# Kernel tuning notes

Measured on AMD Instinct MI355X. Metric: run time of the kernel, lower is better.

## Reference

```python
import jax, jax.numpy as jnp
import numpy as np

N, K_IN, K_OUT = 200000, 8, 4
E, D, H, O = 800000, 64, 128, 1


def setup_inputs() -> dict:
    key = jax.random.key(0)
    ks = jax.random.split(key, 8)
    edges = jax.random.normal(ks[0], (E, D), dtype=jnp.float32)
    in_idx = jax.random.randint(ks[1], (N, K_IN), 0, E, dtype=jnp.int32)
    in_mask = jax.random.randint(ks[2], (N, K_IN), 0, 2, dtype=jnp.int32)
    out_idx = jax.random.randint(ks[3], (N, K_OUT), 0, E, dtype=jnp.int32)
    out_mask = jax.random.randint(ks[4], (N, K_OUT), 0, 2, dtype=jnp.int32)
    # FC stack params: layer0 takes 2*D (edge feat ++ pooled attention context)
    W0 = jax.random.normal(ks[5], (H, 2 * D), dtype=jnp.float32) * (1.0 / np.sqrt(2 * D))
    b0 = jnp.zeros((H,), dtype=jnp.float32)
    W1 = jax.random.normal(ks[6], (H, H), dtype=jnp.float32) * (1.0 / np.sqrt(H))
    b1 = jnp.zeros((H,), dtype=jnp.float32)
    Wout = jax.random.normal(ks[7], (O, H), dtype=jnp.float32) * (1.0 / np.sqrt(H))
    bout = jnp.zeros((O,), dtype=jnp.float32)
    return {"edges": edges, "in_idx": in_idx, "in_mask": in_mask,
            "out_idx": out_idx, "out_mask": out_mask,
            "W0": W0, "b0": b0, "W1": W1, "b1": b1, "Wout": Wout, "bout": bout}


def _forward(edges, in_idx, in_mask, out_idx, out_mask, W0, b0, W1, b1, Wout, bout):
    d = edges.shape[1]
    mbool = in_mask.astype(bool)                       # [N, K_in]
    mf = in_mask.astype(edges.dtype)[..., None]        # [N, K_in, 1]
    # gather per-node in-edge sets: [N, K_in, D]
    Ein = edges[in_idx]
    # self-attention over the in-edge set (query=key=value=in_edges)
    scores = jnp.einsum('nqd,nkd->nqk', Ein, Ein) / jnp.sqrt(jnp.asarray(d, edges.dtype))
    scores = jnp.where(mbool[:, None, :], scores, jnp.asarray(-1e9, edges.dtype))
    attn = jax.nn.softmax(scores, axis=-1)
    att_out = jnp.einsum('nqk,nkd->nqd', attn, Ein)    # [N, K_in, D]
    # pool attended rows over valid queries -> weighted_in_edges [N, D]
    denom = jnp.maximum(mf.sum(axis=1), 1.0)
    pooled = (att_out * mf).sum(axis=1) / denom
    # per out-edge: concat(edge_feat, pooled) -> MLP
    Eout = edges[out_idx]                              # [N, K_out, D]
    pooled_b = jnp.broadcast_to(pooled[:, None, :], Eout.shape)
    x = jnp.concatenate([Eout, pooled_b], axis=-1)     # [N, K_out, 2D]
    h = jax.nn.relu(jnp.einsum('nkd,hd->nkh', x, W0) + b0)
    h = jax.nn.relu(jnp.einsum('nkh,gh->nkg', h, W1) + b1)
    y = jnp.einsum('nkh,oh->nko', h, Wout) + bout      # [N, K_out, O]
    y = y * out_mask.astype(y.dtype)[..., None]        # zero padded out-edges
    return y.reshape(-1, y.shape[-1])                  # [N*K_out, O]


def reference(edges, in_idx, in_mask, out_idx, out_mask, W0, b0, W1, b1, Wout, bout):
    return _forward(edges, in_idx, in_mask, out_idx, out_mask, W0, b0, W1, b1, Wout, bout)
```

## Files before the change

### kernel.cpp

```cpp
#include <hip/hip_runtime.h>
#include <math.h>

#define D 64
#define H 128
#define KIN 8
#define KOUT 4
#define NPB 16
#define ROWS (NPB*KOUT)
#define THREADS 256
#define WAVES 4
#define NPW (NPB/WAVES)
#define XLDB 136
#define ELD16 72

typedef __attribute__((ext_vector_type(8))) short short8v;
typedef __attribute__((ext_vector_type(4))) float f32x4;

__device__ inline unsigned short f2bf(float f) {
    union { float f; unsigned u; } v; v.f = f;
    unsigned r = v.u + 0x7FFF + ((v.u >> 16) & 1);
    return (unsigned short)(r >> 16);
}

__global__ void convert_w_kernel(const float* __restrict__ W0,
                                 const float* __restrict__ W1,
                                 unsigned short* __restrict__ Wbf) {
    const int i = blockIdx.x * 256 + threadIdx.x;
    const float v = (i < H*H) ? W0[i] : W1[i - H*H];
    Wbf[i] = f2bf(v);
}

__global__ __launch_bounds__(THREADS, 4) void encoder_kernel(
    const float* __restrict__ edges,
    const int*   __restrict__ in_idx,
    const int*   __restrict__ in_mask,
    const int*   __restrict__ out_idx,
    const int*   __restrict__ out_mask,
    const float* __restrict__ b0, const float* __restrict__ b1,
    const float* __restrict__ Wout, const float* __restrict__ bout,
    const unsigned short* __restrict__ Wbf,
    float* __restrict__ out, int N)
{
    __shared__ __align__(16) unsigned short xbuf[ROWS][XLDB];
    __shared__ __align__(16) unsigned short eins[WAVES][16][ELD16];
    __shared__ float omaskf[ROWS];

    const int tid  = threadIdx.x;
    const int wave = tid >> 6;
    const int lane = tid & 63;
    const int nodeBase = blockIdx.x * NPB;

    const int col = lane & 15;
    const int grp = lane >> 4;

    for (int it = 0; it < 2; ++it) {
        const int nl0 = wave * NPW + it * 2;
        const int n0  = nodeBase + nl0;

        const int   idx_l  = in_idx [n0*KIN  + col];
        const float mkcol  = (float)in_mask[n0*KIN  + col];
        const int   oidx_l = out_idx[n0*KOUT + (lane & 7)];

        float ein_r[16];
        #pragma unroll
        for (int r = 0; r < 16; ++r) {
            const int gi = __shfl(idx_l, r);
            ein_r[r] = edges[(size_t)gi * D + lane];
            eins[wave][r][lane] = f2bf(ein_r[r]);
        }
        #pragma unroll
        for (int r = 0; r < 8; ++r) {
            const int gi = __shfl(oidx_l, r);
            xbuf[nl0*KOUT + r][lane] = f2bf(edges[(size_t)gi * D + lane]);
        }
        if (lane < 2*KOUT) omaskf[nl0*KOUT + lane] = (float)out_mask[n0*KOUT + lane];

        const short8v f0 = *(const short8v*)&eins[wave][col][grp*8];
        const short8v f1 = *(const short8v*)&eins[wave][col][32 + grp*8];
        f32x4 sc = (f32x4){0.f, 0.f, 0.f, 0.f};
        sc = __builtin_amdgcn_mfma_f32_16x16x32_bf16(f0, f0, sc, 0, 0, 0);
        sc = __builtin_amdgcn_mfma_f32_16x16x32_bf16(f1, f1, sc, 0, 0, 0);

        float s0, s1, s2, s3;
        {
            const bool kv = (mkcol > 0.f);
            #define MSK(jj, sv) { const int row = grp*4 + jj; \
                const bool ok = kv && ((row < 8) == (col < 8)); \
                sv = ok ? sc[jj] * 0.125f : -1e9f; }
            MSK(0, s0) MSK(1, s1) MSK(2, s2) MSK(3, s3)
            #undef MSK
        }
        float m0=s0, m1=s1, m2=s2, m3=s3;
        #pragma unroll
        for (int off = 1; off < 16; off <<= 1) {
            m0 = fmaxf(m0, __shfl_xor(m0, off));
            m1 = fmaxf(m1, __shfl_xor(m1, off));
            m2 = fmaxf(m2, __shfl_xor(m2, off));
            m3 = fmaxf(m3, __shfl_xor(m3, off));
        }
        float e0=__expf(s0-m0), e1=__expf(s1-m1), e2=__expf(s2-m2), e3=__expf(s3-m3);
        float t0=e0, t1=e1, t2=e2, t3=e3;
        #pragma unroll
        for (int off = 1; off < 16; off <<= 1) {
            t0 += __shfl_xor(t0, off); t1 += __shfl_xor(t1, off);
            t2 += __shfl_xor(t2, off); t3 += __shfl_xor(t3, off);
        }
        float wsum = __shfl(mkcol, grp*4 + 0) * (e0 / t0)
                   + __shfl(mkcol, grp*4 + 1) * (e1 / t1)
                   + __shfl(mkcol, grp*4 + 2) * (e2 / t2)
                   + __shfl(mkcol, grp*4 + 3) * (e3 / t3);
        wsum += __shfl_xor(wsum, 16);
        wsum += __shfl_xor(wsum, 32);

        float dn = mkcol;
        dn += __shfl_xor(dn, 1); dn += __shfl_xor(dn, 2); dn += __shfl_xor(dn, 4);
        const float dnA = fmaxf(__shfl(dn, 0), 1.f);
        const float dnB = fmaxf(__shfl(dn, 8), 1.f);

        float pA = 0.f, pB = 0.f;
        #pragma unroll
        for (int k = 0; k < 8; ++k) {
            pA += __shfl(wsum, k)     * ein_r[k];
            pB += __shfl(wsum, 8 + k) * ein_r[8 + k];
        }
        const unsigned short pbA = f2bf(pA / dnA);
        const unsigned short pbB = f2bf(pB / dnB);
        #pragma unroll
        for (int j = 0; j < KOUT; ++j) {
            xbuf[ nl0   *KOUT + j][D + lane] = pbA;
            xbuf[(nl0+1)*KOUT + j][D + lane] = pbB;
        }
    }
    __syncthreads();

    const int rowbase = (wave >> 1) * 32;
    const int colbase = (wave & 1) * 64;
    const int l15  = lane & 15;
    const int kofs = (lane >> 4) * 8;
    const int rrow = (lane >> 4) * 4;

    #pragma unroll
    for (int layer = 0; layer < 2; ++layer) {
        const unsigned short* __restrict__ Wl = Wbf + layer * (H*H);
        const float* __restrict__ bl = layer ? b1 : b0;

        f32x4 acc[2][4];
        #pragma unroll
        for (int ct = 0; ct < 4; ++ct) {
            const float bv = bl[colbase + ct*16 + l15];
            #pragma unroll
            for (int r = 0; r < 2; ++r) acc[r][ct] = (f32x4){bv, bv, bv, bv};
        }

        #pragma unroll
        for (int ks = 0; ks < 4; ++ks) {
            short8v bf[4];
            #pragma unroll
            for (int ct = 0; ct < 4; ++ct)
                bf[ct] = *(const short8v*)&Wl[(size_t)(colbase + ct*16 + l15) * H + ks*32 + kofs];
            #pragma unroll
            for (int r = 0; r < 2; ++r) {
                const short8v a = *(const short8v*)&xbuf[rowbase + r*16 + l15][ks*32 + kofs];
                #pragma unroll
                for (int ct = 0; ct < 4; ++ct)
                    acc[r][ct] = __builtin_amdgcn_mfma_f32_16x16x32_bf16(a, bf[ct], acc[r][ct], 0, 0, 0);
            }
        }
        __syncthreads();
        #pragma unroll
        for (int r = 0; r < 2; ++r)
            #pragma unroll
            for (int ct = 0; ct < 4; ++ct)
                #pragma unroll
                for (int j = 0; j < 4; ++j)
                    xbuf[rowbase + r*16 + rrow + j][colbase + ct*16 + l15] =
                        f2bf(fmaxf(acc[r][ct][j], 0.f));
        __syncthreads();
    }

    {
        const int row = tid >> 2;
        const int kq  = tid & 3;
        float p = 0.f;
        #pragma unroll
        for (int m = 0; m < 4; ++m) {
            const int k0 = kq*32 + m*8;
            const short8v hv = *(const short8v*)&xbuf[row][k0];
            const float4 w0 = *(const float4*)&Wout[k0];
            const float4 w1 = *(const float4*)&Wout[k0 + 4];
            union { unsigned u; float f; } c;
            float acc8 = 0.f;
            c.u = ((unsigned)(unsigned short)hv[0]) << 16; acc8 += c.f * w0.x;
            c.u = ((unsigned)(unsigned short)hv[1]) << 16; acc8 += c.f * w0.y;
            c.u = ((unsigned)(unsigned short)hv[2]) << 16; acc8 += c.f * w0.z;
            c.u = ((unsigned)(unsigned short)hv[3]) << 16; acc8 += c.f * w0.w;
            c.u = ((unsigned)(unsigned short)hv[4]) << 16; acc8 += c.f * w1.x;
            c.u = ((unsigned)(unsigned short)hv[5]) << 16; acc8 += c.f * w1.y;
            c.u = ((unsigned)(unsigned short)hv[6]) << 16; acc8 += c.f * w1.z;
            c.u = ((unsigned)(unsigned short)hv[7]) << 16; acc8 += c.f * w1.w;
            p += acc8;
        }
        p += __shfl_xor(p, 1);
        p += __shfl_xor(p, 2);
        if (kq == 0) {
            const long long grow = (long long)nodeBase * KOUT + row;
            if (grow < (long long)N * KOUT)
                out[grow] = (p + bout[0]) * omaskf[row];
        }
    }
}

extern "C" void kernel_launch(void* const* d_in, const int* in_sizes, int n_in,
                              void* d_out, int out_size, void* d_ws, size_t ws_size,
                              hipStream_t stream)
{
    const float* edges  = (const float*)d_in[0];
    const int* in_idx   = (const int*)d_in[1];
    const int* in_mask  = (const int*)d_in[2];
    const int* out_idx  = (const int*)d_in[3];
    const int* out_mask = (const int*)d_in[4];
    const float* W0   = (const float*)d_in[5];
    const float* b0   = (const float*)d_in[6];
    const float* W1   = (const float*)d_in[7];
    const float* b1   = (const float*)d_in[8];
    const float* Wout = (const float*)d_in[9];
    const float* bout = (const float*)d_in[10];
    float* out = (float*)d_out;
    unsigned short* Wbf = (unsigned short*)d_ws;

    const int nNodes = in_sizes[1] / KIN;
    convert_w_kernel<<<(2*H*H + 255) / 256, 256, 0, stream>>>(W0, W1, Wbf);
    const int grid = (nNodes + NPB - 1) / NPB;
    encoder_kernel<<<grid, THREADS, 0, stream>>>(
        edges, in_idx, in_mask, out_idx, out_mask,
        b0, b1, Wout, bout, Wbf, out, nNodes);
}
```

Baseline: 643.7 us.

## Make each wave own its 16 MLP rows, removing block barriers and batching gathers

Each wave now handles its 4 nodes end to end. It keeps a private 16-row activation tile and computes all 128 output columns itself, so every __syncthreads in the MLP stage is gone. All 48 edge-row gathers are issued up front before any compute to expose more memory-level parallelism. Occupancy is raised via launch bounds and a smaller LDS stride. The trade-offs are that each wave loads the full weight matrices from global/L2 with no sharing across waves, and more registers are live during the gathers.

```diff
diff --git a/kernel.cpp b/kernel.cpp
--- a/kernel.cpp
+++ b/kernel.cpp
@@ -5,12 +5,9 @@
 #define H 128
 #define KIN 8
 #define KOUT 4
-#define NPB 16
-#define ROWS (NPB*KOUT)
 #define THREADS 256
 #define WAVES 4
-#define NPW (NPB/WAVES)
-#define XLDB 136
+#define XLDB 132
 #define ELD16 72
 
 typedef __attribute__((ext_vector_type(8))) short short8v;
@@ -30,7 +27,7 @@
     Wbf[i] = f2bf(v);
 }
 
-__global__ __launch_bounds__(THREADS, 4) void encoder_kernel(
+__global__ __launch_bounds__(THREADS, 6) void encoder_kernel(
     const float* __restrict__ edges,
     const int*   __restrict__ in_idx,
     const int*   __restrict__ in_mask,
@@ -41,40 +38,37 @@
     const unsigned short* __restrict__ Wbf,
     float* __restrict__ out, int N)
 {
-    __shared__ __align__(16) unsigned short xbuf[ROWS][XLDB];
+    __shared__ __align__(16) unsigned short xbuf[WAVES][16][XLDB];
     __shared__ __align__(16) unsigned short eins[WAVES][16][ELD16];
-    __shared__ float omaskf[ROWS];
 
     const int tid  = threadIdx.x;
     const int wave = tid >> 6;
     const int lane = tid & 63;
-    const int nodeBase = blockIdx.x * NPB;
-
-    const int col = lane & 15;
-    const int grp = lane >> 4;
-
-    for (int it = 0; it < 2; ++it) {
-        const int nl0 = wave * NPW + it * 2;
-        const int n0  = nodeBase + nl0;
-
-        const int   idx_l  = in_idx [n0*KIN  + col];
-        const float mkcol  = (float)in_mask[n0*KIN  + col];
-        const int   oidx_l = out_idx[n0*KOUT + (lane & 7)];
-
-        float ein_r[16];
-        #pragma unroll
-        for (int r = 0; r < 16; ++r) {
-            const int gi = __shfl(idx_l, r);
-            ein_r[r] = edges[(size_t)gi * D + lane];
-            eins[wave][r][lane] = f2bf(ein_r[r]);
-        }
-        #pragma unroll
-        for (int r = 0; r < 8; ++r) {
-            const int gi = __shfl(oidx_l, r);
-            xbuf[nl0*KOUT + r][lane] = f2bf(edges[(size_t)gi * D + lane]);
-        }
-        if (lane < 2*KOUT) omaskf[nl0*KOUT + lane] = (float)out_mask[n0*KOUT + lane];
-
+    const int col  = lane & 15;
+    const int grp  = lane >> 4;
+    const int n0   = blockIdx.x * 16 + wave * 4;
+
+    const int   idxA = in_idx [(size_t)(n0+0)*KIN + col];
+    const int   idxB = in_idx [(size_t)(n0+2)*KIN + col];
+    const float mkA  = (float)in_mask[(size_t)(n0+0)*KIN + col];
+    const float mkB  = (float)in_mask[(size_t)(n0+2)*KIN + col];
+    const int   oidx = out_idx[(size_t)n0*KOUT + col];
+    const float omsk = (float)out_mask[(size_t)n0*KOUT + (lane >> 2)];
+
+    float einA[16], einB[16], eout[16];
+    #pragma unroll
+    for (int r = 0; r < 16; ++r) einA[r] = edges[(size_t)__shfl(idxA, r) * D + lane];
+    #pragma unroll
+    for (int r = 0; r < 16; ++r) einB[r] = edges[(size_t)__shfl(idxB, r) * D + lane];
+    #pragma unroll
+    for (int r = 0; r < 16; ++r) eout[r] = edges[(size_t)__shfl(oidx, r) * D + lane];
+
+    #pragma unroll
+    for (int r = 0; r < 16; ++r) xbuf[wave][r][lane] = f2bf(eout[r]);
+
+    auto do_pair = [&](const float* einr, const float mkcol, const int xrow0) {
+        #pragma unroll
+        for (int r = 0; r < 16; ++r) eins[wave][r][lane] = f2bf(einr[r]);
         const short8v f0 = *(const short8v*)&eins[wave][col][grp*8];
         const short8v f1 = *(const short8v*)&eins[wave][col][32 + grp*8];
         f32x4 sc = (f32x4){0.f, 0.f, 0.f, 0.f};
@@ -120,72 +114,56 @@
         float pA = 0.f, pB = 0.f;
         #pragma unroll
         for (int k = 0; k < 8; ++k) {
-            pA += __shfl(wsum, k)     * ein_r[k];
-            pB += __shfl(wsum, 8 + k) * ein_r[8 + k];
+            pA += __shfl(wsum, k)     * einr[k];
+            pB += __shfl(wsum, 8 + k) * einr[8 + k];
         }
         const unsigned short pbA = f2bf(pA / dnA);
         const unsigned short pbB = f2bf(pB / dnB);
         #pragma unroll
         for (int j = 0; j < KOUT; ++j) {
-            xbuf[ nl0   *KOUT + j][D + lane] = pbA;
-            xbuf[(nl0+1)*KOUT + j][D + lane] = pbB;
-        }
-    }
-    __syncthreads();
-
-    const int rowbase = (wave >> 1) * 32;
-    const int colbase = (wave & 1) * 64;
-    const int l15  = lane & 15;
-    const int kofs = (lane >> 4) * 8;
-    const int rrow = (lane >> 4) * 4;
-
+            xbuf[wave][xrow0 + j]    [D + lane] = pbA;
+            xbuf[wave][xrow0 + 4 + j][D + lane] = pbB;
+        }
+    };
+    do_pair(einA, mkA, 0);
+    do_pair(einB, mkB, 8);
+
+    const int kofs = grp * 8;
     #pragma unroll
     for (int layer = 0; layer < 2; ++layer) {
         const unsigned short* __restrict__ Wl = Wbf + layer * (H*H);
         const float* __restrict__ bl = layer ? b1 : b0;
 
-        f32x4 acc[2][4];
-        #pragma unroll
-        for (int ct = 0; ct < 4; ++ct) {
-            const float bv = bl[colbase + ct*16 + l15];
+        f32x4 acc[8];
+        #pragma unroll
+        for (int ct = 0; ct < 8; ++ct) {
+            const float bv = bl[ct*16 + col];
+            acc[ct] = (f32x4){bv, bv, bv, bv};
+        }
+        #pragma unroll
+        for (int ks = 0; ks < 4; ++ks) {
+            const short8v a = *(const short8v*)&xbuf[wave][col][ks*32 + kofs];
             #pragma unroll
-            for (int r = 0; r < 2; ++r) acc[r][ct] = (f32x4){bv, bv, bv, bv};
-        }
-
-        #pragma unroll
-        for (int ks = 0; ks < 4; ++ks) {
-            short8v bf[4];
+            for (int ct = 0; ct < 8; ++ct) {
+                const short8v bf = *(const short8v*)&Wl[(size_t)(ct*16 + col)*H + ks*32 + kofs];
+                acc[ct] = __builtin_amdgcn_mfma_f32_16x16x32_bf16(a, bf, acc[ct], 0, 0, 0);
+            }
+        }
+        #pragma unroll
+        for (int ct = 0; ct < 8; ++ct)
             #pragma unroll
-            for (int ct = 0; ct < 4; ++ct)
-                bf[ct] = *(const short8v*)&Wl[(size_t)(colbase + ct*16 + l15) * H + ks*32 + kofs];
-            #pragma unroll
-            for (int r = 0; r < 2; ++r) {
-                const short8v a = *(const short8v*)&xbuf[rowbase + r*16 + l15][ks*32 + kofs];
-                #pragma unroll
-                for (int ct = 0; ct < 4; ++ct)
-                    acc[r][ct] = __builtin_amdgcn_mfma_f32_16x16x32_bf16(a, bf[ct], acc[r][ct], 0, 0, 0);
-            }
-        }
-        __syncthreads();
-        #pragma unroll
-        for (int r = 0; r < 2; ++r)
-            #pragma unroll
-            for (int ct = 0; ct < 4; ++ct)
-                #pragma unroll
-                for (int j = 0; j < 4; ++j)
-                    xbuf[rowbase + r*16 + rrow + j][colbase + ct*16 + l15] =
-                        f2bf(fmaxf(acc[r][ct][j], 0.f));
-        __syncthreads();
+            for (int j = 0; j < 4; ++j)
+                xbuf[wave][grp*4 + j][ct*16 + col] = f2bf(fmaxf(acc[ct][j], 0.f));
     }
 
     {
-        const int row = tid >> 2;
-        const int kq  = tid & 3;
+        const int row = lane >> 2;
+        const int kq  = lane & 3;
         float p = 0.f;
         #pragma unroll
         for (int m = 0; m < 4; ++m) {
             const int k0 = kq*32 + m*8;
-            const short8v hv = *(const short8v*)&xbuf[row][k0];
+            const short8v hv = *(const short8v*)&xbuf[wave][row][k0];
             const float4 w0 = *(const float4*)&Wout[k0];
             const float4 w1 = *(const float4*)&Wout[k0 + 4];
             union { unsigned u; float f; } c;
@@ -203,9 +181,9 @@
         p += __shfl_xor(p, 1);
         p += __shfl_xor(p, 2);
         if (kq == 0) {
-            const long long grow = (long long)nodeBase * KOUT + row;
+            const long long grow = (long long)n0 * KOUT + row;
             if (grow < (long long)N * KOUT)
-                out[grow] = (p + bout[0]) * omaskf[row];
+                out[grow] = (p + bout[0]) * omsk;
         }
     }
 }
@@ -230,7 +208,7 @@
 
     const int nNodes = in_sizes[1] / KIN;
     convert_w_kernel<<<(2*H*H + 255) / 256, 256, 0, stream>>>(W0, W1, Wbf);
-    const int grid = (nNodes + NPB - 1) / NPB;
+    const int grid = (nNodes + 15) / 16;
     encoder_kernel<<<grid, THREADS, 0, stream>>>(
         edges, in_idx, in_mask, out_idx, out_mask,
         b0, b1, Wout, bout, Wbf, out, nNodes);
```

New measurement: 688.2 us. +6.9%, slower.

## Split fused encoder into separate attention and MLP kernels via workspace buffer

Applied to the files above, without the earlier changes.

The single fused kernel is split in two. An attention kernel computes pooled in-edge context per node and writes it as bf16 to workspace. An MLP kernel then gathers out-edge features plus the pooled vectors and runs the FC stack on 128-row tiles instead of 64. The split lets each stage pick its own occupancy and gives the MLP larger MFMA tiles that reuse weight fragments more, at the cost of an extra round trip of pooled data through global memory and possibly several chunked launches when workspace is small.

```diff
diff --git a/kernel.cpp b/kernel.cpp
--- a/kernel.cpp
+++ b/kernel.cpp
@@ -5,13 +5,9 @@
 #define H 128
 #define KIN 8
 #define KOUT 4
-#define NPB 16
-#define ROWS (NPB*KOUT)
-#define THREADS 256
-#define WAVES 4
-#define NPW (NPB/WAVES)
+#define ELD16 72
 #define XLDB 136
-#define ELD16 72
+#define BROWS 128
 
 typedef __attribute__((ext_vector_type(8))) short short8v;
 typedef __attribute__((ext_vector_type(4))) float f32x4;
@@ -30,183 +26,184 @@
     Wbf[i] = f2bf(v);
 }
 
-__global__ __launch_bounds__(THREADS, 4) void encoder_kernel(
+__global__ __launch_bounds__(256, 6) void attn_kernel(
     const float* __restrict__ edges,
     const int*   __restrict__ in_idx,
     const int*   __restrict__ in_mask,
+    unsigned short* __restrict__ pooled,
+    int nodeBase, int nodeEnd)
+{
+    __shared__ __align__(16) unsigned short eins[4][16][ELD16];
+    const int tid  = threadIdx.x;
+    const int wave = tid >> 6;
+    const int lane = tid & 63;
+    const int col  = lane & 15;
+    const int grp  = lane >> 4;
+    const int n0   = nodeBase + blockIdx.x * 8 + wave * 2;
+    if (n0 >= nodeEnd) return;
+
+    const int   idx_l = in_idx [(size_t)n0*KIN + col];
+    const float mkcol = (float)in_mask[(size_t)n0*KIN + col];
+
+    float ein_r[16];
+    #pragma unroll
+    for (int r = 0; r < 16; ++r)
+        ein_r[r] = edges[(size_t)__shfl(idx_l, r) * D + lane];
+    #pragma unroll
+    for (int r = 0; r < 16; ++r) eins[wave][r][lane] = f2bf(ein_r[r]);
+
+    const short8v f0 = *(const short8v*)&eins[wave][col][grp*8];
+    const short8v f1 = *(const short8v*)&eins[wave][col][32 + grp*8];
+    f32x4 sc = (f32x4){0.f, 0.f, 0.f, 0.f};
+    sc = __builtin_amdgcn_mfma_f32_16x16x32_bf16(f0, f0, sc, 0, 0, 0);
+    sc = __builtin_amdgcn_mfma_f32_16x16x32_bf16(f1, f1, sc, 0, 0, 0);
+
+    float s0, s1, s2, s3;
+    {
+        const bool kv = (mkcol > 0.f);
+        #define MSK(jj, sv) { const int row = grp*4 + jj; \
+            const bool ok = kv && ((row < 8) == (col < 8)); \
+            sv = ok ? sc[jj] * 0.125f : -1e9f; }
+        MSK(0, s0) MSK(1, s1) MSK(2, s2) MSK(3, s3)
+        #undef MSK
+    }
+    float m0=s0, m1=s1, m2=s2, m3=s3;
+    #pragma unroll
+    for (int off = 1; off < 16; off <<= 1) {
+        m0 = fmaxf(m0, __shfl_xor(m0, off));
+        m1 = fmaxf(m1, __shfl_xor(m1, off));
+        m2 = fmaxf(m2, __shfl_xor(m2, off));
+        m3 = fmaxf(m3, __shfl_xor(m3, off));
+    }
+    float e0=__expf(s0-m0), e1=__expf(s1-m1), e2=__expf(s2-m2), e3=__expf(s3-m3);
+    float t0=e0, t1=e1, t2=e2, t3=e3;
+    #pragma unroll
+    for (int off = 1; off < 16; off <<= 1) {
+        t0 += __shfl_xor(t0, off); t1 += __shfl_xor(t1, off);
+        t2 += __shfl_xor(t2, off); t3 += __shfl_xor(t3, off);
+    }
+    float wsum = __shfl(mkcol, grp*4 + 0) * (e0 / t0)
+               + __shfl(mkcol, grp*4 + 1) * (e1 / t1)
+               + __shfl(mkcol, grp*4 + 2) * (e2 / t2)
+               + __shfl(mkcol, grp*4 + 3) * (e3 / t3);
+    wsum += __shfl_xor(wsum, 16);
+    wsum += __shfl_xor(wsum, 32);
+
+    float dn = mkcol;
+    dn += __shfl_xor(dn, 1); dn += __shfl_xor(dn, 2); dn += __shfl_xor(dn, 4);
+    const float dnA = fmaxf(__shfl(dn, 0), 1.f);
+    const float dnB = fmaxf(__shfl(dn, 8), 1.f);
+
+    float pA = 0.f, pB = 0.f;
+    #pragma unroll
+    for (int k = 0; k < 8; ++k) {
+        pA += __shfl(wsum, k)     * ein_r[k];
+        pB += __shfl(wsum, 8 + k) * ein_r[8 + k];
+    }
+    const size_t pbase = (size_t)(n0 - nodeBase) * D;
+    pooled[pbase + lane]     = f2bf(pA / dnA);
+    pooled[pbase + D + lane] = f2bf(pB / dnB);
+}
+
+__global__ __launch_bounds__(256, 4) void mlp_kernel(
+    const float* __restrict__ edges,
     const int*   __restrict__ out_idx,
     const int*   __restrict__ out_mask,
     const float* __restrict__ b0, const float* __restrict__ b1,
     const float* __restrict__ Wout, const float* __restrict__ bout,
     const unsigned short* __restrict__ Wbf,
-    float* __restrict__ out, int N)
+    const unsigned short* __restrict__ pooled,
+    float* __restrict__ out,
+    int nodeBase, int nodeEnd)
 {
-    __shared__ __align__(16) unsigned short xbuf[ROWS][XLDB];
-    __shared__ __align__(16) unsigned short eins[WAVES][16][ELD16];
-    __shared__ float omaskf[ROWS];
-
+    __shared__ __align__(16) unsigned short xbuf[BROWS][XLDB];
     const int tid  = threadIdx.x;
     const int wave = tid >> 6;
     const int lane = tid & 63;
-    const int nodeBase = blockIdx.x * NPB;
-
-    const int col = lane & 15;
-    const int grp = lane >> 4;
-
-    for (int it = 0; it < 2; ++it) {
-        const int nl0 = wave * NPW + it * 2;
-        const int n0  = nodeBase + nl0;
-
-        const int   idx_l  = in_idx [n0*KIN  + col];
-        const float mkcol  = (float)in_mask[n0*KIN  + col];
-        const int   oidx_l = out_idx[n0*KOUT + (lane & 7)];
-
-        float ein_r[16];
-        #pragma unroll
-        for (int r = 0; r < 16; ++r) {
-            const int gi = __shfl(idx_l, r);
-            ein_r[r] = edges[(size_t)gi * D + lane];
-            eins[wave][r][lane] = f2bf(ein_r[r]);
-        }
-        #pragma unroll
-        for (int r = 0; r < 8; ++r) {
-            const int gi = __shfl(oidx_l, r);
-            xbuf[nl0*KOUT + r][lane] = f2bf(edges[(size_t)gi * D + lane]);
-        }
-        if (lane < 2*KOUT) omaskf[nl0*KOUT + lane] = (float)out_mask[n0*KOUT + lane];
-
-        const short8v f0 = *(const short8v*)&eins[wave][col][grp*8];
-        const short8v f1 = *(const short8v*)&eins[wave][col][32 + grp*8];
-        f32x4 sc = (f32x4){0.f, 0.f, 0.f, 0.f};
-        sc = __builtin_amdgcn_mfma_f32_16x16x32_bf16(f0, f0, sc, 0, 0, 0);
-        sc = __builtin_amdgcn_mfma_f32_16x16x32_bf16(f1, f1, sc, 0, 0, 0);
-
-        float s0, s1, s2, s3;
-        {
-            const bool kv = (mkcol > 0.f);
-            #define MSK(jj, sv) { const int row = grp*4 + jj; \
-                const bool ok = kv && ((row < 8) == (col < 8)); \
-                sv = ok ? sc[jj] * 0.125f : -1e9f; }
-            MSK(0, s0) MSK(1, s1) MSK(2, s2) MSK(3, s3)
-            #undef MSK
-        }
-        float m0=s0, m1=s1, m2=s2, m3=s3;
-        #pragma unroll
-        for (int off = 1; off < 16; off <<= 1) {
-            m0 = fmaxf(m0, __shfl_xor(m0, off));
-            m1 = fmaxf(m1, __shfl_xor(m1, off));
-            m2 = fmaxf(m2, __shfl_xor(m2, off));
-            m3 = fmaxf(m3, __shfl_xor(m3, off));
-        }
-        float e0=__expf(s0-m0), e1=__expf(s1-m1), e2=__expf(s2-m2), e3=__expf(s3-m3);
-        float t0=e0, t1=e1, t2=e2, t3=e3;
-        #pragma unroll
-        for (int off = 1; off < 16; off <<= 1) {
-            t0 += __shfl_xor(t0, off); t1 += __shfl_xor(t1, off);
-            t2 += __shfl_xor(t2, off); t3 += __shfl_xor(t3, off);
-        }
-        float wsum = __shfl(mkcol, grp*4 + 0) * (e0 / t0)
-                   + __shfl(mkcol, grp*4 + 1) * (e1 / t1)
-                   + __shfl(mkcol, grp*4 + 2) * (e2 / t2)
-                   + __shfl(mkcol, grp*4 + 3) * (e3 / t3);
-        wsum += __shfl_xor(wsum, 16);
-        wsum += __shfl_xor(wsum, 32);
-
-        float dn = mkcol;
-        dn += __shfl_xor(dn, 1); dn += __shfl_xor(dn, 2); dn += __shfl_xor(dn, 4);
-        const float dnA = fmaxf(__shfl(dn, 0), 1.f);
-        const float dnB = fmaxf(__shfl(dn, 8), 1.f);
-
-        float pA = 0.f, pB = 0.f;
-        #pragma unroll
-        for (int k = 0; k < 8; ++k) {
-            pA += __shfl(wsum, k)     * ein_r[k];
-            pB += __shfl(wsum, 8 + k) * ein_r[8 + k];
-        }
-        const unsigned short pbA = f2bf(pA / dnA);
-        const unsigned short pbB = f2bf(pB / dnB);
-        #pragma unroll
-        for (int j = 0; j < KOUT; ++j) {
-            xbuf[ nl0   *KOUT + j][D + lane] = pbA;
-            xbuf[(nl0+1)*KOUT + j][D + lane] = pbB;
+    const int rowBase = (nodeBase + blockIdx.x * 32) * KOUT;
+    const int rowEnd  = nodeEnd * KOUT;
+
+    #pragma unroll 4
+    for (int rr = 0; rr < 32; ++rr) {
+        const int row  = wave * 32 + rr;
+        const int grow = rowBase + row;
+        if (grow < rowEnd) {
+            const int n  = grow >> 2;
+            const int oi = out_idx[grow];
+            xbuf[row][lane]     = f2bf(edges[(size_t)oi * D + lane]);
+            xbuf[row][D + lane] = pooled[(size_t)(n - nodeBase) * D + lane];
         }
     }
     __syncthreads();
 
-    const int rowbase = (wave >> 1) * 32;
-    const int colbase = (wave & 1) * 64;
     const int l15  = lane & 15;
     const int kofs = (lane >> 4) * 8;
     const int rrow = (lane >> 4) * 4;
+    const int rowb = (wave >> 1) * 64;
+    const int colb = (wave & 1) * 64;
 
     #pragma unroll
     for (int layer = 0; layer < 2; ++layer) {
         const unsigned short* __restrict__ Wl = Wbf + layer * (H*H);
         const float* __restrict__ bl = layer ? b1 : b0;
 
-        f32x4 acc[2][4];
+        f32x4 acc[4][4];
         #pragma unroll
         for (int ct = 0; ct < 4; ++ct) {
-            const float bv = bl[colbase + ct*16 + l15];
-            #pragma unroll
-            for (int r = 0; r < 2; ++r) acc[r][ct] = (f32x4){bv, bv, bv, bv};
-        }
-
+            const float bv = bl[colb + ct*16 + l15];
+            #pragma unroll
+            for (int rt = 0; rt < 4; ++rt) acc[rt][ct] = (f32x4){bv, bv, bv, bv};
+        }
         #pragma unroll
         for (int ks = 0; ks < 4; ++ks) {
-            short8v bf[4];
+            short8v bfr[4];
             #pragma unroll
             for (int ct = 0; ct < 4; ++ct)
-                bf[ct] = *(const short8v*)&Wl[(size_t)(colbase + ct*16 + l15) * H + ks*32 + kofs];
-            #pragma unroll
-            for (int r = 0; r < 2; ++r) {
-                const short8v a = *(const short8v*)&xbuf[rowbase + r*16 + l15][ks*32 + kofs];
+                bfr[ct] = *(const short8v*)&Wl[(size_t)(colb + ct*16 + l15) * H + ks*32 + kofs];
+            #pragma unroll
+            for (int rt = 0; rt < 4; ++rt) {
+                const short8v a = *(const short8v*)&xbuf[rowb + rt*16 + l15][ks*32 + kofs];
                 #pragma unroll
                 for (int ct = 0; ct < 4; ++ct)
-                    acc[r][ct] = __builtin_amdgcn_mfma_f32_16x16x32_bf16(a, bf[ct], acc[r][ct], 0, 0, 0);
+                    acc[rt][ct] = __builtin_amdgcn_mfma_f32_16x16x32_bf16(a, bfr[ct], acc[rt][ct], 0, 0, 0);
             }
         }
         __syncthreads();
         #pragma unroll
-        for (int r = 0; r < 2; ++r)
+        for (int rt = 0; rt < 4; ++rt)
             #pragma unroll
             for (int ct = 0; ct < 4; ++ct)
                 #pragma unroll
                 for (int j = 0; j < 4; ++j)
-                    xbuf[rowbase + r*16 + rrow + j][colbase + ct*16 + l15] =
-                        f2bf(fmaxf(acc[r][ct][j], 0.f));
+                    xbuf[rowb + rt*16 + rrow + j][colb + ct*16 + l15] =
+                        f2bf(fmaxf(acc[rt][ct][j], 0.f));
         __syncthreads();
     }
 
     {
-        const int row = tid >> 2;
-        const int kq  = tid & 3;
+        const int row = tid >> 1;
+        const int kh  = tid & 1;
         float p = 0.f;
         #pragma unroll
-        for (int m = 0; m < 4; ++m) {
-            const int k0 = kq*32 + m*8;
+        for (int m = 0; m < 8; ++m) {
+            const int k0 = kh*64 + m*8;
             const short8v hv = *(const short8v*)&xbuf[row][k0];
             const float4 w0 = *(const float4*)&Wout[k0];
             const float4 w1 = *(const float4*)&Wout[k0 + 4];
             union { unsigned u; float f; } c;
-            float acc8 = 0.f;
-            c.u = ((unsigned)(unsigned short)hv[0]) << 16; acc8 += c.f * w0.x;
-            c.u = ((unsigned)(unsigned short)hv[1]) << 16; acc8 += c.f * w0.y;
-            c.u = ((unsigned)(unsigned short)hv[2]) << 16; acc8 += c.f * w0.z;
-            c.u = ((unsigned)(unsigned short)hv[3]) << 16; acc8 += c.f * w0.w;
-            c.u = ((unsigned)(unsigned short)hv[4]) << 16; acc8 += c.f * w1.x;
-            c.u = ((unsigned)(unsigned short)hv[5]) << 16; acc8 += c.f * w1.y;
-            c.u = ((unsigned)(unsigned short)hv[6]) << 16; acc8 += c.f * w1.z;
-            c.u = ((unsigned)(unsigned short)hv[7]) << 16; acc8 += c.f * w1.w;
-            p += acc8;
+            c.u = ((unsigned)(unsigned short)hv[0]) << 16; p += c.f * w0.x;
+            c.u = ((unsigned)(unsigned short)hv[1]) << 16; p += c.f * w0.y;
+            c.u = ((unsigned)(unsigned short)hv[2]) << 16; p += c.f * w0.z;
+            c.u = ((unsigned)(unsigned short)hv[3]) << 16; p += c.f * w0.w;
+            c.u = ((unsigned)(unsigned short)hv[4]) << 16; p += c.f * w1.x;
+            c.u = ((unsigned)(unsigned short)hv[5]) << 16; p += c.f * w1.y;
+            c.u = ((unsigned)(unsigned short)hv[6]) << 16; p += c.f * w1.z;
+            c.u = ((unsigned)(unsigned short)hv[7]) << 16; p += c.f * w1.w;
         }
         p += __shfl_xor(p, 1);
-        p += __shfl_xor(p, 2);
-        if (kq == 0) {
-            const long long grow = (long long)nodeBase * KOUT + row;
-            if (grow < (long long)N * KOUT)
-                out[grow] = (p + bout[0]) * omaskf[row];
-        }
+        const int grow = rowBase + row;
+        if (kh == 0 && grow < rowEnd)
+            out[grow] = (p + bout[0]) * (float)out_mask[grow];
     }
 }
 
@@ -226,12 +223,26 @@
     const float* Wout = (const float*)d_in[9];
     const float* bout = (const float*)d_in[10];
     float* out = (float*)d_out;
-    unsigned short* Wbf = (unsigned short*)d_ws;
+
+    unsigned short* Wbf       = (unsigned short*)d_ws;
+    unsigned short* pooledBuf = (unsigned short*)((char*)d_ws + 65536);
 
     const int nNodes = in_sizes[1] / KIN;
     convert_w_kernel<<<(2*H*H + 255) / 256, 256, 0, stream>>>(W0, W1, Wbf);
-    const int grid = (nNodes + NPB - 1) / NPB;
-    encoder_kernel<<<grid, THREADS, 0, stream>>>(
-        edges, in_idx, in_mask, out_idx, out_mask,
-        b0, b1, Wout, bout, Wbf, out, nNodes);
-}
+
+    const size_t avail = (ws_size > 65536) ? ws_size - 65536 : 0;
+    long long maxNodes = (long long)(avail / (D * sizeof(unsigned short)));
+    int chunk = (int)((maxNodes / 32) * 32);
+    if (chunk <= 0) chunk = 32;
+    if (chunk > nNodes) chunk = nNodes;
+
+    for (int base = 0; base < nNodes; base += chunk) {
+        const int end = (base + chunk < nNodes) ? base + chunk : nNodes;
+        const int cn  = end - base;
+        attn_kernel<<<(cn + 7) / 8, 256, 0, stream>>>(
+            edges, in_idx, in_mask, pooledBuf, base, end);
+        mlp_kernel<<<(cn + 31) / 32, 256, 0, stream>>>(
+            edges, out_idx, out_mask, b0, b1, Wout, bout,
+            Wbf, pooledBuf, out, base, end);
+    }
+}
```

Result: faster. 588.0 us (-8.7%).
